# Kernel optimization log

Hardware: AMD Instinct MI355X
Metric: run time of the kernel (lower is better)

The kernel has to match this reference:

```python
import jax, jax.numpy as jnp
import numpy as np

K = 20      # neighbors per node
D_T = 32    # timestep embedding dim

def _timestep_embedding(t, dim):
    half = dim // 2
    freqs = jnp.exp(-jnp.log(10000.0) * jnp.arange(half, dtype=jnp.float32) / (half - 1))
    args = t[:, None] * freqs[None, :]
    return jnp.concatenate([jnp.sin(args), jnp.cos(args)], axis=-1)

def _knn(pos, k):
    # pos: [N,3] -> (sources, targets): [N*k] edge index lists
    r2 = jnp.sum(pos * pos, axis=-1)
    d2 = r2[:, None] + r2[None, :] - 2.0 * (pos @ pos.T)   # [N,N] squared distances
    n = pos.shape[0]
    d2 = d2 + 1e10 * jnp.eye(n, dtype=pos.dtype)           # exclude self
    d2 = jax.lax.stop_gradient(d2)                         # indices only, no grad path
    _, idx = jax.lax.top_k(-d2, k)                         # [N,k]
    targets = jnp.repeat(jnp.arange(n), k)
    sources = idx.reshape(-1)
    return sources, targets

def _forward(z, t, conditioning, Wc1, bc1, Wc2, bc2, Wc3, bc3, We1, be1, We2, be2, Wn1, bn1, Wn2, bn2, alpha, beta):
    B, N, _ = z.shape
    pos, vel, massf = z[..., :3], z[..., 3:6], z[..., 6:]
    t = t * jnp.ones((B,), z.dtype)
    temb = _timestep_embedding(t, D_T)                     # [B,32]
    cond = jnp.concatenate([temb, conditioning], axis=1)   # [B,36]
    h = jax.nn.gelu(cond @ Wc1 + bc1)
    h = jax.nn.gelu(h @ Wc2 + bc2)
    cond = h @ Wc3 + bc3                                   # [B,36]
    fs = massf + cond[:, None, :]                          # scalar node feats [B,N,36]

    def single(pos_b, vel_b, fs_b):
        src, tgt = _knn(pos_b, K)
        rel = pos_b[src] - pos_b[tgt]                      # [E,3]
        r2 = jnp.sum(rel * rel, axis=-1, keepdims=True)
        vs, vt = vel_b[src], vel_b[tgt]
        # rotation-invariant edge features
        inv = jnp.concatenate([
            fs_b[src], fs_b[tgt], r2,
            jnp.sum(vs * vt, -1, keepdims=True),
            jnp.sum(vs * rel, -1, keepdims=True),
            jnp.sum(vt * rel, -1, keepdims=True),
        ], axis=-1)                                        # [E,76]
        e = jax.nn.gelu(inv @ We1 + be1) @ We2 + be2       # [E,4]
        logit, smsg, c_rel, c_vel = e[:, 0], e[:, 1], e[:, 2], e[:, 3]
        # segment softmax over incoming edges of each target node
        m = jax.ops.segment_max(logit, tgt, num_segments=N)
        a = jnp.exp(logit - m[tgt])
        denom = jax.ops.segment_sum(a, tgt, num_segments=N)
        w = a / denom[tgt]
        # equivariant vector messages, invariant scalar messages
        vmsg = w[:, None] * (c_rel[:, None] * rel + c_vel[:, None] * vs)
        vagg = jax.ops.segment_sum(vmsg, tgt, num_segments=N)              # [N,3]
        sagg = jax.ops.segment_sum(w * smsg, tgt, num_segments=N)[:, None]  # [N,1]
        hn = jax.nn.gelu(jnp.concatenate([fs_b, sagg], axis=-1) @ Wn1 + bn1)
        sout = hn @ Wn2 + bn2                              # [N,1] 0e output
        pos_out = pos_b + alpha * vagg                     # 1o
        feat_out = jnp.concatenate([beta * vagg, sout], axis=-1)  # 1o + 0e
        return jnp.concatenate([pos_out, feat_out], axis=-1)      # [N,7]

    h_all = jax.vmap(single)(pos, vel, fs)
    return z + h_all

def setup_inputs():
    key = jax.random.key(0)
    ks = jax.random.split(key, 10)
    B, N = 2, 8192
    d_cond = D_T + 4          # 36
    e_in = 2 * d_cond + 4     # 76
    e_hid, n_hid = 128, 64
    g = lambda i, shp: jax.random.normal(ks[i], shp, jnp.float32) * 0.05
    return {
        "z": jax.random.normal(ks[0], (B, N, 7), jnp.float32),
        "t": jax.random.uniform(ks[1], (B,), jnp.float32),
        "conditioning": jax.random.normal(ks[2], (B, 4), jnp.float32),
        "mask": jnp.ones((B, N), dtype=bool),
        "Wc1": g(3, (d_cond, 4 * d_cond)), "bc1": jnp.zeros((4 * d_cond,), jnp.float32),
        "Wc2": g(4, (4 * d_cond, 4 * d_cond)), "bc2": jnp.zeros((4 * d_cond,), jnp.float32),
        "Wc3": g(5, (4 * d_cond, d_cond)), "bc3": jnp.zeros((d_cond,), jnp.float32),
        "We1": g(6, (e_in, e_hid)), "be1": jnp.zeros((e_hid,), jnp.float32),
        "We2": g(7, (e_hid, 4)), "be2": jnp.zeros((4,), jnp.float32),
        "Wn1": g(8, (d_cond + 1, n_hid)), "bn1": jnp.zeros((n_hid,), jnp.float32),
        "Wn2": g(9, (n_hid, 1)), "bn2": jnp.zeros((1,), jnp.float32),
        "alpha": jnp.float32(0.1), "beta": jnp.float32(0.1),
    }

def reference(z, t, conditioning, mask, Wc1, bc1, Wc2, bc2, Wc3, bc3, We1, be1, We2, be2, Wn1, bn1, Wn2, bn2, alpha, beta):
    # mask is unused (module docstring: does not support masking)
    return _forward(z, t, conditioning, Wc1, bc1, Wc2, bc2, Wc3, bc3, We1, be1, We2, be2, Wn1, bn1, Wn2, bn2, alpha, beta)
```

## Files before the change

kernel.cpp:

```cpp
#include <hip/hip_runtime.h>
#include <math.h>

#define NB 8192
#define BATCH 2
#define KNN 20
#define BN (BATCH*NB)
#define NE (BN*KNN)
#define GT 16
#define NG 8
#define BIG 3.0e38f

__device__ __forceinline__ float gelu_f(float x){
    float x3 = x*x*x;
    float a = 0.7978845608028654f*(x + 0.044715f*x3);
    float e2 = __expf(2.0f*a);
    float th = 1.0f - __fdividef(2.0f, e2+1.0f);
    return 0.5f*x*(1.0f+th);
}

__global__ __launch_bounds__(256) void prepcond_kernel(const float* __restrict__ z,
        const float* __restrict__ t,
        const float* __restrict__ conditioning,
        const float* __restrict__ Wc1, const float* __restrict__ bc1,
        const float* __restrict__ Wc2, const float* __restrict__ bc2,
        const float* __restrict__ Wc3, const float* __restrict__ bc3,
        const float* __restrict__ We1, const float* __restrict__ be1,
        const float* __restrict__ We2,
        const float* __restrict__ Wn1, const float* __restrict__ bn1,
        float4* __restrict__ pos4, float4* __restrict__ vel4,
        float* __restrict__ consts, float* __restrict__ pack){
    int tid = threadIdx.x;
    int g = blockIdx.x*256 + tid;
    const float* zp = z + (size_t)g*7;
    float x = zp[0], y = zp[1], zz = zp[2];
    float r2 = x*x + y*y + zz*zz;
    pos4[g] = make_float4(x, y, zz, r2);
    vel4[g] = make_float4(zp[3], zp[4], zp[5], zp[6]);

    if (blockIdx.x >= BATCH) return;
    int b = blockIdx.x;
    __shared__ float ci[36];
    __shared__ float h1[144];
    __shared__ float h2[144];
    __shared__ float cnd[36];
    float tv = t[b];
    if (tid < 16){
        float f = expf(-9.210340371976184f * (float)tid / 15.0f);
        float a = tv*f;
        ci[tid]    = sinf(a);
        ci[16+tid] = cosf(a);
    }
    if (tid < 4) ci[32+tid] = conditioning[b*4+tid];
    __syncthreads();
    if (tid < 144){
        float acc = bc1[tid];
        #pragma unroll
        for (int c=0;c<36;c++) acc += ci[c]*Wc1[c*144+tid];
        h1[tid] = gelu_f(acc);
    }
    __syncthreads();
    if (tid < 144){
        float acc = bc2[tid];
        #pragma unroll 36
        for (int c=0;c<144;c++) acc += h1[c]*Wc2[c*144+tid];
        h2[tid] = gelu_f(acc);
    }
    __syncthreads();
    if (tid < 36){
        float acc = bc3[tid];
        #pragma unroll 36
        for (int c=0;c<144;c++) acc += h2[c]*Wc3[c*36+tid];
        cnd[tid] = acc;
    }
    __syncthreads();
    if (tid < 128){
        float accC = be1[tid], s1 = 0.f, s2 = 0.f;
        #pragma unroll
        for (int c=0;c<36;c++){
            float w1 = We1[c*128+tid];
            float w2 = We1[(36+c)*128+tid];
            accC += cnd[c]*(w1+w2);
            s1 += w1; s2 += w2;
        }
        consts[b*128+tid] = accC;
        pack[tid*12 + b] = accC;
        if (b==0){
            consts[256+tid] = s1; consts[384+tid] = s2;
            pack[tid*12+2] = s1;
            pack[tid*12+3] = s2;
            pack[tid*12+4] = We1[72*128+tid];
            pack[tid*12+5] = We1[73*128+tid];
            pack[tid*12+6] = We1[74*128+tid];
            pack[tid*12+7] = We1[75*128+tid];
            pack[tid*12+8]  = We2[tid*4+0];
            pack[tid*12+9]  = We2[tid*4+1];
            pack[tid*12+10] = We2[tid*4+2];
            pack[tid*12+11] = We2[tid*4+3];
        }
    }
    if (tid < 64){
        float accD = bn1[tid], t1 = 0.f;
        #pragma unroll
        for (int c=0;c<36;c++){
            float w = Wn1[c*64+tid];
            accD += cnd[c]*w;
            t1 += w;
        }
        consts[512 + b*64 + tid] = accD;
        if (b==0) consts[640+tid] = t1;
    }
}

__global__ __launch_bounds__(512, 4) void knn_kernel(const float4* __restrict__ pos4,
                                                     int* __restrict__ nbr){
    __shared__ float4 sPos[GT*64];
    __shared__ float2 sCand[32*64];
    int tid = threadIdx.x;
    int w = tid >> 6, lane = tid & 63;
    int n0g = blockIdx.x * 32;
    int b = n0g >> 13;
    int n0 = n0g & (NB-1);
    const float4* __restrict__ P = pos4 + b*NB;

    int nw = n0 + w*4;
    float nx[4], ny[4], nz[4], pw[4], acc[4];
    #pragma unroll
    for (int k=0;k<4;k++){
        float4 p = P[nw+k];
        nx[k] = -2.0f*p.x; ny[k] = -2.0f*p.y; nz[k] = -2.0f*p.z; pw[k] = p.w;
        acc[k] = BIG;
    }
    int selfTile = n0 >> 6;
    int sl0 = (n0 & 63) + w*4;

    float4 pre0 = P[(w*2    )*64 + lane];
    float4 pre1 = P[(w*2 + 1)*64 + lane];
    for (int g=0; g<NG; ++g){
        __syncthreads();
        sPos[(w*2    )*64 + lane] = pre0;
        sPos[(w*2 + 1)*64 + lane] = pre1;
        if (g+1 < NG){
            pre0 = P[((g+1)*GT + w*2    )*64 + lane];
            pre1 = P[((g+1)*GT + w*2 + 1)*64 + lane];
        }
        __syncthreads();
        int tbase = g*GT;
        #pragma unroll
        for (int t=0;t<GT;t++){
            float4 q = sPos[t*64 + lane];
            if (tbase + t != selfTile){
                #pragma unroll
                for (int k=0;k<4;k++){
                    float d2 = fmaf(nx[k],q.x, fmaf(ny[k],q.y, fmaf(nz[k],q.z, pw[k]+q.w)));
                    acc[k] = fminf(acc[k], d2);
                }
            } else {
                #pragma unroll
                for (int k=0;k<4;k++){
                    float d2 = fmaf(nx[k],q.x, fmaf(ny[k],q.y, fmaf(nz[k],q.z, pw[k]+q.w)));
                    if (lane == sl0 + k) d2 = BIG;
                    acc[k] = fminf(acc[k], d2);
                }
            }
        }
    }

    float T[4];
    #pragma unroll
    for (int k=0;k<4;k++){
        float v = acc[k];
        #pragma unroll
        for (int K=2; K<=64; K<<=1){
            #pragma unroll
            for (int j=K>>1; j>0; j>>=1){
                float o = __shfl_xor(v, j);
                bool keepmin = (((lane & j) == 0) == ((lane & K) == 0));
                float mn = fminf(v,o), mx = fmaxf(v,o);
                v = keepmin ? mn : mx;
            }
        }
        T[k] = __shfl(v, 19);
    }

    int cnt[4];
    #pragma unroll
    for (int k=0;k<4;k++) cnt[k] = 0;
    unsigned long long lt = (1ull << lane) - 1ull;

    pre0 = P[(w*2    )*64 + lane];
    pre1 = P[(w*2 + 1)*64 + lane];
    for (int g=0; g<NG; ++g){
        __syncthreads();
        sPos[(w*2    )*64 + lane] = pre0;
        sPos[(w*2 + 1)*64 + lane] = pre1;
        if (g+1 < NG){
            pre0 = P[((g+1)*GT + w*2    )*64 + lane];
            pre1 = P[((g+1)*GT + w*2 + 1)*64 + lane];
        }
        __syncthreads();
        int tbase = g*GT;
        #pragma unroll 4
        for (int t=0;t<GT;t++){
            int tile = tbase + t;
            float4 q = sPos[t*64 + lane];
            int j = (tile<<6) + lane;
            bool selft = (tile == selfTile);
            #pragma unroll
            for (int k=0;k<4;k++){
                float d2 = fmaf(nx[k],q.x, fmaf(ny[k],q.y, fmaf(nz[k],q.z, pw[k]+q.w)));
                bool hit = (d2 <= T[k]);
                if (selft && (lane == sl0 + k)) hit = false;
                unsigned long long m = __ballot(hit);
                if (m){
                    if (hit){
                        int off = cnt[k] + (int)__popcll(m & lt);
                        if (off < 64)
                            sCand[(w*4+k)*64 + off] = make_float2(d2, __int_as_float(j));
                    }
                    cnt[k] += (int)__popcll(m);
                }
            }
        }
    }

    #pragma unroll
    for (int k=0;k<4;k++){
        int m = cnt[k]; if (m > 64) m = 64;
        float d; int idx;
        if (lane < m){
            float2 e = sCand[(w*4+k)*64 + lane];
            d = e.x; idx = __float_as_int(e.y);
        } else { d = BIG; idx = 0x7f000000 + lane; }
        #pragma unroll
        for (int K=2; K<=64; K<<=1){
            #pragma unroll
            for (int j=K>>1; j>0; j>>=1){
                float od = __shfl_xor(d, j);
                int   oi = __shfl_xor(idx, j);
                bool pless = (od < d) || (od == d && oi < idx);
                bool keepmin = (((lane & j) == 0) == ((lane & K) == 0));
                if (pless == keepmin){ d = od; idx = oi; }
            }
        }
        if (lane < KNN) nbr[(size_t)(n0g + w*4 + k)*KNN + lane] = idx;
    }
}

__global__ __launch_bounds__(320) void edgenode_kernel(const float4* __restrict__ pos4,
        const float4* __restrict__ vel4,
        const int* __restrict__ nbr,
        const float* __restrict__ pack,
        const float* __restrict__ consts,
        const float* __restrict__ Wn1,
        const float* __restrict__ Wn2,
        const float* __restrict__ be2,
        const float* __restrict__ bn2,
        const float* __restrict__ alpha_p,
        const float* __restrict__ beta_p,
        const float* __restrict__ z,
        float* __restrict__ out){
    __shared__ float4 sP[384];
    __shared__ float sLg[320], sSm[320], sUx[320], sUy[320], sUz[320];
    __shared__ float sD[64], sT1[64], sW36[64], sWo[64];
    __shared__ float sMf[16];
    __shared__ float4 sAgg[16];
    __shared__ float sPart[320];

    int tid = threadIdx.x;
    bool bb = (blockIdx.x >= 512);
    for (int k=tid; k<384; k+=320) sP[k] = ((const float4*)pack)[k];
    if (tid < 64){
        sD[tid]   = consts[512 + (bb?64:0) + tid];
        sT1[tid]  = consts[640+tid];
        sW36[tid] = Wn1[36*64+tid];
        sWo[tid]  = Wn2[tid];
    }

    int e = blockIdx.x*320 + tid;
    int i = e / KNN;
    int ln = tid / KNN;
    int r  = tid - ln*KNN;
    int bbase = bb ? NB : 0;
    int s = nbr[e];
    float4 ps = pos4[bbase + s], pt = pos4[i];
    float4 vs = vel4[bbase + s], vt = vel4[i];
    if (r == 0) sMf[ln] = vt.w;

    float rx = ps.x - pt.x, ry = ps.y - pt.y, rz = ps.z - pt.z;
    float r2  = rx*rx + ry*ry + rz*rz;
    float vv  = vs.x*vt.x + vs.y*vt.y + vs.z*vt.z;
    float vsr = vs.x*rx + vs.y*ry + vs.z*rz;
    float vtr = vt.x*rx + vt.y*ry + vt.z*rz;
    float mfs = vs.w, mft = vt.w;
    __syncthreads();

    float a0 = be2[0], a1 = be2[1], a2 = be2[2], a3 = be2[3];
    #pragma unroll 4
    for (int h=0; h<128; h++){
        float4 A  = sP[h*3];
        float4 Bv = sP[h*3+1];
        float4 C  = sP[h*3+2];
        float base = bb ? A.y : A.x;
        float x = base + mfs*A.z + mft*A.w + r2*Bv.x + vv*Bv.y + vsr*Bv.z + vtr*Bv.w;
        float gx = gelu_f(x);
        a0 += gx*C.x; a1 += gx*C.y; a2 += gx*C.z; a3 += gx*C.w;
    }
    sLg[tid] = a0;
    sSm[tid] = a1;
    sUx[tid] = a2*rx + a3*vs.x;
    sUy[tid] = a2*ry + a3*vs.y;
    sUz[tid] = a2*rz + a3*vs.z;
    __syncthreads();

    if (tid < 16){
        int base = tid*KNN;
        float m = -BIG;
        #pragma unroll
        for (int q=0;q<KNN;q++) m = fmaxf(m, sLg[base+q]);
        float den=0.f, wx=0.f, wy=0.f, wz=0.f, wsm=0.f;
        #pragma unroll
        for (int q=0;q<KNN;q++){
            float a = __expf(sLg[base+q]-m);
            den += a;
            wsm += a*sSm[base+q];
            wx  += a*sUx[base+q];
            wy  += a*sUy[base+q];
            wz  += a*sUz[base+q];
        }
        float inv = __fdividef(1.0f, den);
        sAgg[tid] = make_float4(wx*inv, wy*inv, wz*inv, wsm*inv);
    }
    __syncthreads();

    {
        float mf = sMf[ln];
        float sg = sAgg[ln].w;
        float part = 0.f;
        #pragma unroll
        for (int h=r; h<64; h+=KNN){
            float x = sD[h] + mf*sT1[h] + sg*sW36[h];
            part += gelu_f(x)*sWo[h];
        }
        sPart[tid] = part;
    }
    __syncthreads();

    if (tid < 16){
        float sout = bn2[0];
        #pragma unroll
        for (int q=0;q<KNN;q++) sout += sPart[tid*KNN+q];
        int node = blockIdx.x*16 + tid;
        float alpha = alpha_p[0], beta = beta_p[0];
        float4 ag = sAgg[tid];
        const float* zp = z + (size_t)node*7;
        float* op = out + (size_t)node*7;
        op[0] = zp[0]*2.0f + alpha*ag.x;
        op[1] = zp[1]*2.0f + alpha*ag.y;
        op[2] = zp[2]*2.0f + alpha*ag.z;
        op[3] = zp[3] + beta*ag.x;
        op[4] = zp[4] + beta*ag.y;
        op[5] = zp[5] + beta*ag.z;
        op[6] = zp[6] + sout;
    }
}

extern "C" void kernel_launch(void* const* d_in, const int* in_sizes, int n_in,
                              void* d_out, int out_size, void* d_ws, size_t ws_size,
                              hipStream_t stream) {
    const float* z    = (const float*)d_in[0];
    const float* t    = (const float*)d_in[1];
    const float* cond = (const float*)d_in[2];
    const float* Wc1  = (const float*)d_in[4];
    const float* bc1  = (const float*)d_in[5];
    const float* Wc2  = (const float*)d_in[6];
    const float* bc2  = (const float*)d_in[7];
    const float* Wc3  = (const float*)d_in[8];
    const float* bc3  = (const float*)d_in[9];
    const float* We1  = (const float*)d_in[10];
    const float* be1  = (const float*)d_in[11];
    const float* We2  = (const float*)d_in[12];
    const float* be2  = (const float*)d_in[13];
    const float* Wn1  = (const float*)d_in[14];
    const float* bn1  = (const float*)d_in[15];
    const float* Wn2  = (const float*)d_in[16];
    const float* bn2  = (const float*)d_in[17];
    const float* alp  = (const float*)d_in[18];
    const float* bet  = (const float*)d_in[19];
    float* out = (float*)d_out;

    char* ws = (char*)d_ws;
    float4* pos4   = (float4*)(ws);
    float4* vel4   = (float4*)(ws + 262144);
    float*  consts = (float*)(ws + 524288);
    float*  pack   = (float*)(ws + 528384);
    int*    nbr    = (int*)(ws + 534528);

    prepcond_kernel<<<dim3(BN/256), dim3(256), 0, stream>>>(z, t, cond,
        Wc1, bc1, Wc2, bc2, Wc3, bc3, We1, be1, We2, Wn1, bn1,
        pos4, vel4, consts, pack);
    knn_kernel<<<dim3(BN/32), dim3(512), 0, stream>>>(pos4, nbr);
    edgenode_kernel<<<dim3(BN/16), dim3(320), 0, stream>>>(pos4, vel4, nbr, pack, consts,
        Wn1, Wn2, be2, bn2, alp, bet, z, out);
}
```

Measured before the change: 208.5 us.

## Increase per-thread work in kNN and edge kernels for register reuse

The kNN kernel now runs 4 waves of 256 threads, each handling 8 query nodes instead of 4, so every shared-memory position load feeds twice as many distance evaluations. The edge/node kernel processes 4 edges per thread (64 nodes per block), so each weight-pack load from shared memory is reused across four edges. The per-block batch select is also folded into the pack load. The intent is to cut LDS traffic and loop overhead per FLOP, at the cost of higher register pressure, larger shared-memory footprint and fewer blocks/waves in flight.

Result: slower. 256.8 us (+23.2%).

```diff
diff --git a/kernel.cpp b/kernel.cpp
--- a/kernel.cpp
+++ b/kernel.cpp
@@ -111,7 +111,7 @@
     }
 }
 
-__global__ __launch_bounds__(512, 4) void knn_kernel(const float4* __restrict__ pos4,
+__global__ __launch_bounds__(256, 2) void knn_kernel(const float4* __restrict__ pos4,
                                                      int* __restrict__ nbr){
     __shared__ float4 sPos[GT*64];
     __shared__ float2 sCand[32*64];
@@ -122,41 +122,47 @@
     int n0 = n0g & (NB-1);
     const float4* __restrict__ P = pos4 + b*NB;
 
-    int nw = n0 + w*4;
-    float nx[4], ny[4], nz[4], pw[4], acc[4];
-    #pragma unroll
-    for (int k=0;k<4;k++){
+    int nw = n0 + w*8;
+    float nx[8], ny[8], nz[8], pw[8], acc[8];
+    #pragma unroll
+    for (int k=0;k<8;k++){
         float4 p = P[nw+k];
         nx[k] = -2.0f*p.x; ny[k] = -2.0f*p.y; nz[k] = -2.0f*p.z; pw[k] = p.w;
         acc[k] = BIG;
     }
     int selfTile = n0 >> 6;
-    int sl0 = (n0 & 63) + w*4;
-
-    float4 pre0 = P[(w*2    )*64 + lane];
-    float4 pre1 = P[(w*2 + 1)*64 + lane];
+    int sl0 = (n0 & 63) + w*8;
+
+    float4 pre0 = P[(w*4    )*64 + lane];
+    float4 pre1 = P[(w*4 + 1)*64 + lane];
+    float4 pre2 = P[(w*4 + 2)*64 + lane];
+    float4 pre3 = P[(w*4 + 3)*64 + lane];
     for (int g=0; g<NG; ++g){
         __syncthreads();
-        sPos[(w*2    )*64 + lane] = pre0;
-        sPos[(w*2 + 1)*64 + lane] = pre1;
+        sPos[(w*4    )*64 + lane] = pre0;
+        sPos[(w*4 + 1)*64 + lane] = pre1;
+        sPos[(w*4 + 2)*64 + lane] = pre2;
+        sPos[(w*4 + 3)*64 + lane] = pre3;
         if (g+1 < NG){
-            pre0 = P[((g+1)*GT + w*2    )*64 + lane];
-            pre1 = P[((g+1)*GT + w*2 + 1)*64 + lane];
+            pre0 = P[((g+1)*GT + w*4    )*64 + lane];
+            pre1 = P[((g+1)*GT + w*4 + 1)*64 + lane];
+            pre2 = P[((g+1)*GT + w*4 + 2)*64 + lane];
+            pre3 = P[((g+1)*GT + w*4 + 3)*64 + lane];
         }
         __syncthreads();
         int tbase = g*GT;
-        #pragma unroll
+        #pragma unroll 4
         for (int t=0;t<GT;t++){
             float4 q = sPos[t*64 + lane];
             if (tbase + t != selfTile){
                 #pragma unroll
-                for (int k=0;k<4;k++){
+                for (int k=0;k<8;k++){
                     float d2 = fmaf(nx[k],q.x, fmaf(ny[k],q.y, fmaf(nz[k],q.z, pw[k]+q.w)));
                     acc[k] = fminf(acc[k], d2);
                 }
             } else {
                 #pragma unroll
-                for (int k=0;k<4;k++){
+                for (int k=0;k<8;k++){
                     float d2 = fmaf(nx[k],q.x, fmaf(ny[k],q.y, fmaf(nz[k],q.z, pw[k]+q.w)));
                     if (lane == sl0 + k) d2 = BIG;
                     acc[k] = fminf(acc[k], d2);
@@ -165,9 +171,9 @@
         }
     }
 
-    float T[4];
-    #pragma unroll
-    for (int k=0;k<4;k++){
+    float T[8];
+    #pragma unroll
+    for (int k=0;k<8;k++){
         float v = acc[k];
         #pragma unroll
         for (int K=2; K<=64; K<<=1){
@@ -182,31 +188,37 @@
         T[k] = __shfl(v, 19);
     }
 
-    int cnt[4];
-    #pragma unroll
-    for (int k=0;k<4;k++) cnt[k] = 0;
+    int cnt[8];
+    #pragma unroll
+    for (int k=0;k<8;k++) cnt[k] = 0;
     unsigned long long lt = (1ull << lane) - 1ull;
 
-    pre0 = P[(w*2    )*64 + lane];
-    pre1 = P[(w*2 + 1)*64 + lane];
+    pre0 = P[(w*4    )*64 + lane];
+    pre1 = P[(w*4 + 1)*64 + lane];
+    pre2 = P[(w*4 + 2)*64 + lane];
+    pre3 = P[(w*4 + 3)*64 + lane];
     for (int g=0; g<NG; ++g){
         __syncthreads();
-        sPos[(w*2    )*64 + lane] = pre0;
-        sPos[(w*2 + 1)*64 + lane] = pre1;
+        sPos[(w*4    )*64 + lane] = pre0;
+        sPos[(w*4 + 1)*64 + lane] = pre1;
+        sPos[(w*4 + 2)*64 + lane] = pre2;
+        sPos[(w*4 + 3)*64 + lane] = pre3;
         if (g+1 < NG){
-            pre0 = P[((g+1)*GT + w*2    )*64 + lane];
-            pre1 = P[((g+1)*GT + w*2 + 1)*64 + lane];
+            pre0 = P[((g+1)*GT + w*4    )*64 + lane];
+            pre1 = P[((g+1)*GT + w*4 + 1)*64 + lane];
+            pre2 = P[((g+1)*GT + w*4 + 2)*64 + lane];
+            pre3 = P[((g+1)*GT + w*4 + 3)*64 + lane];
         }
         __syncthreads();
         int tbase = g*GT;
-        #pragma unroll 4
+        #pragma unroll 2
         for (int t=0;t<GT;t++){
             int tile = tbase + t;
             float4 q = sPos[t*64 + lane];
             int j = (tile<<6) + lane;
             bool selft = (tile == selfTile);
             #pragma unroll
-            for (int k=0;k<4;k++){
+            for (int k=0;k<8;k++){
                 float d2 = fmaf(nx[k],q.x, fmaf(ny[k],q.y, fmaf(nz[k],q.z, pw[k]+q.w)));
                 bool hit = (d2 <= T[k]);
                 if (selft && (lane == sl0 + k)) hit = false;
@@ -215,7 +227,7 @@
                     if (hit){
                         int off = cnt[k] + (int)__popcll(m & lt);
                         if (off < 64)
-                            sCand[(w*4+k)*64 + off] = make_float2(d2, __int_as_float(j));
+                            sCand[(w*8+k)*64 + off] = make_float2(d2, __int_as_float(j));
                     }
                     cnt[k] += (int)__popcll(m);
                 }
@@ -224,11 +236,11 @@
     }
 
     #pragma unroll
-    for (int k=0;k<4;k++){
+    for (int k=0;k<8;k++){
         int m = cnt[k]; if (m > 64) m = 64;
         float d; int idx;
         if (lane < m){
-            float2 e = sCand[(w*4+k)*64 + lane];
+            float2 e = sCand[(w*8+k)*64 + lane];
             d = e.x; idx = __float_as_int(e.y);
         } else { d = BIG; idx = 0x7f000000 + lane; }
         #pragma unroll
@@ -242,7 +254,7 @@
                 if (pless == keepmin){ d = od; idx = oi; }
             }
         }
-        if (lane < KNN) nbr[(size_t)(n0g + w*4 + k)*KNN + lane] = idx;
+        if (lane < KNN) nbr[(size_t)(n0g + w*8 + k)*KNN + lane] = idx;
     }
 }
 
@@ -260,15 +272,18 @@
         const float* __restrict__ z,
         float* __restrict__ out){
     __shared__ float4 sP[384];
-    __shared__ float sLg[320], sSm[320], sUx[320], sUy[320], sUz[320];
+    __shared__ float sLg[1280], sSm[1280], sUx[1280], sUy[1280], sUz[1280];
     __shared__ float sD[64], sT1[64], sW36[64], sWo[64];
-    __shared__ float sMf[16];
-    __shared__ float4 sAgg[16];
-    __shared__ float sPart[320];
+    __shared__ float4 sAgg[64];
+    __shared__ float sPart[256];
 
     int tid = threadIdx.x;
-    bool bb = (blockIdx.x >= 512);
-    for (int k=tid; k<384; k+=320) sP[k] = ((const float4*)pack)[k];
+    bool bb = (blockIdx.x >= 128);
+    for (int k=tid; k<384; k+=320){
+        float4 v = ((const float4*)pack)[k];
+        if (k % 3 == 0) v.x = bb ? v.y : v.x;
+        sP[k] = v;
+    }
     if (tid < 64){
         sD[tid]   = consts[512 + (bb?64:0) + tid];
         sT1[tid]  = consts[640+tid];
@@ -276,43 +291,57 @@
         sWo[tid]  = Wn2[tid];
     }
 
-    int e = blockIdx.x*320 + tid;
-    int i = e / KNN;
-    int ln = tid / KNN;
-    int r  = tid - ln*KNN;
+    int base_e = blockIdx.x*1280;
     int bbase = bb ? NB : 0;
-    int s = nbr[e];
-    float4 ps = pos4[bbase + s], pt = pos4[i];
-    float4 vs = vel4[bbase + s], vt = vel4[i];
-    if (r == 0) sMf[ln] = vt.w;
-
-    float rx = ps.x - pt.x, ry = ps.y - pt.y, rz = ps.z - pt.z;
-    float r2  = rx*rx + ry*ry + rz*rz;
-    float vv  = vs.x*vt.x + vs.y*vt.y + vs.z*vt.z;
-    float vsr = vs.x*rx + vs.y*ry + vs.z*rz;
-    float vtr = vt.x*rx + vt.y*ry + vt.z*rz;
-    float mfs = vs.w, mft = vt.w;
-    __syncthreads();
-
-    float a0 = be2[0], a1 = be2[1], a2 = be2[2], a3 = be2[3];
+
+    float rx[4],ry[4],rz[4],vsx[4],vsy[4],vsz[4];
+    float r2[4],vv[4],vsr[4],vtr[4],mfs[4],mft[4];
+    #pragma unroll
+    for (int r=0;r<4;r++){
+        int le = tid + 320*r;
+        int i = blockIdx.x*64 + le/KNN;
+        int s = nbr[base_e + le];
+        float4 ps = pos4[bbase + s], pt = pos4[i];
+        float4 vs = vel4[bbase + s], vt = vel4[i];
+        rx[r] = ps.x - pt.x; ry[r] = ps.y - pt.y; rz[r] = ps.z - pt.z;
+        vsx[r] = vs.x; vsy[r] = vs.y; vsz[r] = vs.z;
+        r2[r]  = rx[r]*rx[r] + ry[r]*ry[r] + rz[r]*rz[r];
+        vv[r]  = vs.x*vt.x + vs.y*vt.y + vs.z*vt.z;
+        vsr[r] = vs.x*rx[r] + vs.y*ry[r] + vs.z*rz[r];
+        vtr[r] = vt.x*rx[r] + vt.y*ry[r] + vt.z*rz[r];
+        mfs[r] = vs.w; mft[r] = vt.w;
+    }
+    __syncthreads();
+
+    float b2v0 = be2[0], b2v1 = be2[1], b2v2 = be2[2], b2v3 = be2[3];
+    float a0[4], a1[4], a2[4], a3[4];
+    #pragma unroll
+    for (int r=0;r<4;r++){ a0[r]=b2v0; a1[r]=b2v1; a2[r]=b2v2; a3[r]=b2v3; }
     #pragma unroll 4
     for (int h=0; h<128; h++){
         float4 A  = sP[h*3];
         float4 Bv = sP[h*3+1];
         float4 C  = sP[h*3+2];
-        float base = bb ? A.y : A.x;
-        float x = base + mfs*A.z + mft*A.w + r2*Bv.x + vv*Bv.y + vsr*Bv.z + vtr*Bv.w;
-        float gx = gelu_f(x);
-        a0 += gx*C.x; a1 += gx*C.y; a2 += gx*C.z; a3 += gx*C.w;
-    }
-    sLg[tid] = a0;
-    sSm[tid] = a1;
-    sUx[tid] = a2*rx + a3*vs.x;
-    sUy[tid] = a2*ry + a3*vs.y;
-    sUz[tid] = a2*rz + a3*vs.z;
-    __syncthreads();
-
-    if (tid < 16){
+        #pragma unroll
+        for (int r=0;r<4;r++){
+            float x = A.x + mfs[r]*A.z + mft[r]*A.w
+                    + r2[r]*Bv.x + vv[r]*Bv.y + vsr[r]*Bv.z + vtr[r]*Bv.w;
+            float gx = gelu_f(x);
+            a0[r] += gx*C.x; a1[r] += gx*C.y; a2[r] += gx*C.z; a3[r] += gx*C.w;
+        }
+    }
+    #pragma unroll
+    for (int r=0;r<4;r++){
+        int le = tid + 320*r;
+        sLg[le] = a0[r];
+        sSm[le] = a1[r];
+        sUx[le] = a2[r]*rx[r] + a3[r]*vsx[r];
+        sUy[le] = a2[r]*ry[r] + a3[r]*vsy[r];
+        sUz[le] = a2[r]*rz[r] + a3[r]*vsz[r];
+    }
+    __syncthreads();
+
+    if (tid < 64){
         int base = tid*KNN;
         float m = -BIG;
         #pragma unroll
@@ -332,12 +361,14 @@
     }
     __syncthreads();
 
-    {
-        float mf = sMf[ln];
+    if (tid < 256){
+        int ln = tid >> 2;
+        int h0 = (tid & 3)*16;
+        float mf = vel4[blockIdx.x*64 + ln].w;
         float sg = sAgg[ln].w;
         float part = 0.f;
         #pragma unroll
-        for (int h=r; h<64; h+=KNN){
+        for (int h=h0; h<h0+16; h++){
             float x = sD[h] + mf*sT1[h] + sg*sW36[h];
             part += gelu_f(x)*sWo[h];
         }
@@ -345,11 +376,9 @@
     }
     __syncthreads();
 
-    if (tid < 16){
-        float sout = bn2[0];
-        #pragma unroll
-        for (int q=0;q<KNN;q++) sout += sPart[tid*KNN+q];
-        int node = blockIdx.x*16 + tid;
+    if (tid < 64){
+        float sout = bn2[0] + sPart[tid*4] + sPart[tid*4+1] + sPart[tid*4+2] + sPart[tid*4+3];
+        int node = blockIdx.x*64 + tid;
         float alpha = alpha_p[0], beta = beta_p[0];
         float4 ag = sAgg[tid];
         const float* zp = z + (size_t)node*7;
@@ -398,7 +427,7 @@
     prepcond_kernel<<<dim3(BN/256), dim3(256), 0, stream>>>(z, t, cond,
         Wc1, bc1, Wc2, bc2, Wc3, bc3, We1, be1, We2, Wn1, bn1,
         pos4, vel4, consts, pack);
-    knn_kernel<<<dim3(BN/32), dim3(512), 0, stream>>>(pos4, nbr);
-    edgenode_kernel<<<dim3(BN/16), dim3(320), 0, stream>>>(pos4, vel4, nbr, pack, consts,
+    knn_kernel<<<dim3(BN/32), dim3(256), 0, stream>>>(pos4, nbr);
+    edgenode_kernel<<<dim3(BN/64), dim3(320), 0, stream>>>(pos4, vel4, nbr, pack, consts,
         Wn1, Wn2, be2, bn2, alp, bet, z, out);
 }
```
